# Kernel tuning notes

Hardware: AMD Instinct MI355X
Metric: run time of the kernel (lower is better)

Reference implementation:

```python
import jax, jax.numpy as jnp
import numpy as np

WIDTH = 2048
NUM_HEADS = 16
HEAD_DIM = WIDTH // NUM_HEADS  # 128
ROPE_DIMS = HEAD_DIM // 2      # 64, partial rotary
WINDOW = 512
ROPE_BASE = 10000.0
NEG_INF = -1e9


def apply_rope(x, dims, offset=0, base=ROPE_BASE):
    # x: [B, H, L, hd]; non-traditional (half-split) rotary on first `dims` dims.
    L = x.shape[2]
    half = dims // 2
    pos = (offset + jnp.arange(L)).astype(x.dtype)                     # [L]
    inv_freq = jnp.exp(-jnp.log(jnp.asarray(base, x.dtype)) * (jnp.arange(0, dims, 2).astype(x.dtype) / dims))  # [half]
    theta = pos[:, None] * inv_freq[None, :]                           # [L, half]
    cos = jnp.cos(theta)[None, None]                                   # [1,1,L,half]
    sin = jnp.sin(theta)[None, None]
    x1 = x[..., :half]
    x2 = x[..., half:dims]
    rest = x[..., dims:]
    rx1 = x1 * cos - x2 * sin
    rx2 = x1 * sin + x2 * cos
    return jnp.concatenate([rx1, rx2, rest], axis=-1)


def setup_inputs() -> dict:
    key = jax.random.key(0)
    ks = jax.random.split(key, 6)
    B, L, D, hd = 2, 2048, WIDTH, HEAD_DIM
    x = jax.random.normal(ks[0], (B, L, D), dtype=jnp.float32)
    Wq = jax.random.normal(ks[1], (D, D), dtype=jnp.float32) * 0.02
    Wk = jax.random.normal(ks[2], (D, hd), dtype=jnp.float32) * 0.02
    Wv = jax.random.normal(ks[3], (D, hd), dtype=jnp.float32) * 0.02
    Wo = jax.random.normal(ks[4], (D, D), dtype=jnp.float32) * 0.02
    bo = jax.random.normal(ks[5], (D,), dtype=jnp.float32) * 0.02
    return {"x": x, "Wq": Wq, "Wk": Wk, "Wv": Wv, "Wo": Wo, "bo": bo}


def reference(x, Wq, Wk, Wv, Wo, bo):
    B, L, D = x.shape
    H, hd = NUM_HEADS, HEAD_DIM
    scale = hd ** (-0.5)

    q = (x @ Wq).reshape(B, L, H, hd).transpose(0, 2, 1, 3)   # [B,H,L,hd]
    k = (x @ Wk).reshape(B, L, 1, hd).transpose(0, 2, 1, 3)   # [B,1,L,hd] (MQA)
    v = (x @ Wv).reshape(B, L, 1, hd).transpose(0, 2, 1, 3)

    q = apply_rope(q, ROPE_DIMS)
    k = apply_rope(k, ROPE_DIMS)

    # sliding-window causal mask: attend iff 0 <= i - j < WINDOW
    i = jnp.arange(L)[:, None]
    j = jnp.arange(L)[None, :]
    allowed = (i - j >= 0) & (i - j < WINDOW)                  # [L,L]
    mask = jnp.where(allowed, 0.0, NEG_INF).astype(x.dtype)

    scores = jnp.einsum("bhqd,bkd->bhqk", q, k[:, 0]) * scale  # [B,H,L,L]
    scores = scores + mask[None, None]
    attn = jax.nn.softmax(scores, axis=-1)
    out = jnp.einsum("bhqk,bkd->bhqd", attn, v[:, 0])          # [B,H,L,hd]
    out = out.transpose(0, 2, 1, 3).reshape(B, L, D)
    return out @ Wo + bo
```

## Files before the change

kernel.cpp:

```cpp
#include <hip/hip_runtime.h>
#include <hip/hip_bf16.h>
#include <stdint.h>


typedef float  f32x4  __attribute__((ext_vector_type(4)));
typedef __bf16 bf16x8 __attribute__((ext_vector_type(8)));

#define ASYNC_LD16(gp, lp)                                                     \
  __builtin_amdgcn_global_load_lds(                                            \
      (__attribute__((address_space(1))) void*)(gp),                           \
      (__attribute__((address_space(3))) void*)(lp), 16, 0, 0)

__global__ void cvt_bf16(const float* __restrict__ in,
                         __hip_bfloat16* __restrict__ out, int n4) {
  const int i = blockIdx.x * 256 + threadIdx.x;
  if (i >= n4) return;
  const float4 v = ((const float4*)in)[i];
  __align__(8) __hip_bfloat16 t[4] = {
      __float2bfloat16(v.x), __float2bfloat16(v.y),
      __float2bfloat16(v.z), __float2bfloat16(v.w)};
  *(uint2*)(out + (size_t)i * 4) = *(uint2*)t;
}

__global__ __launch_bounds__(256) void transpose_all(
    const float* __restrict__ Wq, const float* __restrict__ Wk,
    const float* __restrict__ Wv, const float* __restrict__ Wo,
    __hip_bfloat16* __restrict__ wqkvT, __hip_bfloat16* __restrict__ woT) {
  __shared__ float t[32][33];
  const int bid = blockIdx.x;
  const float* src;
  __hip_bfloat16* dst;
  int C, cb, rb;
  if (bid < 4096) {
    src = Wq; dst = wqkvT; C = 2048; cb = bid & 63; rb = bid >> 6;
  } else if (bid < 4352) {
    const int l = bid - 4096;
    src = Wk; dst = wqkvT + 2048ull * 2048; C = 128; cb = l & 3; rb = l >> 2;
  } else if (bid < 4608) {
    const int l = bid - 4352;
    src = Wv; dst = wqkvT + 2176ull * 2048; C = 128; cb = l & 3; rb = l >> 2;
  } else {
    const int l = bid - 4608;
    src = Wo; dst = woT; C = 2048; cb = l & 63; rb = l >> 6;
  }
  const int c0 = cb * 32, r0 = rb * 32;
  const int x = threadIdx.x & 31, y = threadIdx.x >> 5;
#pragma unroll
  for (int i = 0; i < 32; i += 8)
    t[y + i][x] = src[(size_t)(r0 + y + i) * C + c0 + x];
  __syncthreads();
#pragma unroll
  for (int i = 0; i < 32; i += 8)
    dst[(size_t)(c0 + y + i) * 2048 + r0 + x] = __float2bfloat16(t[x][y + i]);
}

__device__ __forceinline__ void gemm_core64(const __bf16* __restrict__ A,
                                            const __bf16* __restrict__ BT,
                                            int K, __bf16* As, __bf16* Bs,
                                            f32x4 (&acc)[4][4]) {
  const int tid = threadIdx.x;
  const int wave = tid >> 6;
  const int lane = tid & 63;
  const int m0 = blockIdx.y * 128;
  const int n0 = blockIdx.x * 128;
  const int wm = (wave & 1) * 64;
  const int wn = (wave >> 1) * 64;
  const int ln = lane & 15;
  const int quad = lane >> 4;
  const int rdoff = (quad ^ ((ln >> 1) & 3)) * 8;

  size_t goff[4];
  int ldsoff[4];
#pragma unroll
  for (int i = 0; i < 4; i++) {
    const int cidx = (wave * 4 + i) * 64 + lane;
    const int p = cidx >> 9;
    const int pidx = cidx & 511;
    const int row = pidx >> 2;
    const int cc = pidx & 3;
    const int cg = cc ^ ((row >> 1) & 3);
    goff[i] = (size_t)row * K + p * 32 + cg * 8;
    ldsoff[i] = (wave * 4 + i) * 512;
  }
  const __bf16* Abase = A + (size_t)m0 * K;
  const __bf16* Bbase = BT + (size_t)n0 * K;

  for (int k0 = 0; k0 < K; k0 += 64) {
#pragma unroll
    for (int i = 0; i < 4; i++)
      ASYNC_LD16(Abase + k0 + goff[i], As + ldsoff[i]);
#pragma unroll
    for (int i = 0; i < 4; i++)
      ASYNC_LD16(Bbase + k0 + goff[i], Bs + ldsoff[i]);
    __syncthreads();
    bf16x8 af[4][2], bf[4][2];
#pragma unroll
    for (int i = 0; i < 4; i++)
#pragma unroll
      for (int p = 0; p < 2; p++)
        af[i][p] = *(const bf16x8*)&As[p * 4096 + (wm + i * 16 + ln) * 32 + rdoff];
#pragma unroll
    for (int j = 0; j < 4; j++)
#pragma unroll
      for (int p = 0; p < 2; p++)
        bf[j][p] = *(const bf16x8*)&Bs[p * 4096 + (wn + j * 16 + ln) * 32 + rdoff];
#pragma unroll
    for (int p = 0; p < 2; p++)
#pragma unroll
      for (int i = 0; i < 4; i++)
#pragma unroll
        for (int j = 0; j < 4; j++)
          acc[i][j] = __builtin_amdgcn_mfma_f32_16x16x32_bf16(af[i][p], bf[j][p],
                                                              acc[i][j], 0, 0, 0);
    __syncthreads();
  }
}

__global__ __launch_bounds__(256) void gemm_qkv(
    const __bf16* __restrict__ A, const __bf16* __restrict__ BT,
    __hip_bfloat16* __restrict__ qd, __hip_bfloat16* __restrict__ kd,
    __hip_bfloat16* __restrict__ vtd, int K) {
  __shared__ __align__(16) __bf16 As[128 * 64];
  __shared__ __align__(16) __bf16 Bs[128 * 64];
  f32x4 acc[4][4];
  const f32x4 zero = {0.f, 0.f, 0.f, 0.f};
#pragma unroll
  for (int i = 0; i < 4; i++)
#pragma unroll
    for (int j = 0; j < 4; j++) acc[i][j] = zero;
  gemm_core64(A, BT, K, As, Bs, acc);

  const int tid = threadIdx.x;
  const int wave = tid >> 6;
  const int lane = tid & 63;
  const int quad = lane >> 4;
  const int ln = lane & 15;
  const int m0 = blockIdx.y * 128;
  const int n0 = blockIdx.x * 128;
  const int wm = (wave & 1) * 64;
  const int wn = (wave >> 1) * 64;

  if (n0 == 2176) {
    const int bb = m0 >> 11;
    const int mloc = m0 & 2047;
#pragma unroll
    for (int i = 0; i < 4; i++) {
      const int rb = mloc + wm + i * 16 + quad * 4;
#pragma unroll
      for (int j = 0; j < 4; j++) {
        const int col = wn + j * 16 + ln;
        __align__(8) __hip_bfloat16 t4[4];
#pragma unroll
        for (int r = 0; r < 4; r++) t4[r] = __float2bfloat16(acc[i][j][r]);
        *(uint2*)(vtd + ((size_t)(bb * 128 + col)) * 2048 + rb) = *(uint2*)t4;
      }
    }
    return;
  }

  __hip_bfloat16* dst;
  int dstride, dcol;
  if (n0 < 2048) {
    dst = qd; dstride = 2048; dcol = n0;
  } else {
    dst = kd; dstride = 128; dcol = 0;
  }
  const bool dorope = (wn == 0);
  float invf0 = 0.f, invf1 = 0.f;
  if (dorope) {
    invf0 = expf(-0.28782313662425574f * (float)ln);
    invf1 = expf(-0.28782313662425574f * (float)(16 + ln));
  }

#pragma unroll
  for (int i = 0; i < 4; i++) {
#pragma unroll
    for (int r = 0; r < 4; r++) {
      const int row = m0 + wm + i * 16 + quad * 4 + r;
      float o0 = acc[i][0][r], o1 = acc[i][1][r];
      float o2 = acc[i][2][r], o3 = acc[i][3][r];
      if (dorope) {
        const float pos = (float)(row & 2047);
        float s0, c0, s1, c1;
        __sincosf(pos * invf0, &s0, &c0);
        __sincosf(pos * invf1, &s1, &c1);
        const float a0 = o0, b0 = o2, a1 = o1, b1 = o3;
        o0 = a0 * c0 - b0 * s0;
        o2 = a0 * s0 + b0 * c0;
        o1 = a1 * c1 - b1 * s1;
        o3 = a1 * s1 + b1 * c1;
      }
      __hip_bfloat16* rp = dst + (size_t)row * dstride + dcol + wn + ln;
      rp[0]  = __float2bfloat16(o0);
      rp[16] = __float2bfloat16(o1);
      rp[32] = __float2bfloat16(o2);
      rp[48] = __float2bfloat16(o3);
    }
  }
}

__global__ __launch_bounds__(256) void gemm_out(
    const __bf16* __restrict__ A, const __bf16* __restrict__ BT,
    float* __restrict__ C, const float* __restrict__ bias, int N, int K) {
  __shared__ __align__(16) __bf16 As[128 * 64];
  __shared__ __align__(16) __bf16 Bs[128 * 64];
  f32x4 acc[4][4];
  const f32x4 zero = {0.f, 0.f, 0.f, 0.f};
#pragma unroll
  for (int i = 0; i < 4; i++)
#pragma unroll
    for (int j = 0; j < 4; j++) acc[i][j] = zero;
  gemm_core64(A, BT, K, As, Bs, acc);

  const int tid = threadIdx.x;
  const int wave = tid >> 6;
  const int lane = tid & 63;
  const int m0 = blockIdx.y * 128;
  const int n0 = blockIdx.x * 128;
  const int wm = (wave & 1) * 64;
  const int wn = (wave >> 1) * 64;
  const int lrow = lane & 15;
#pragma unroll
  for (int j = 0; j < 4; j++) {
    const int col = n0 + wn + j * 16 + lrow;
    const float bv = bias[col];
#pragma unroll
    for (int i = 0; i < 4; i++) {
#pragma unroll
      for (int r = 0; r < 4; r++) {
        const int row = m0 + wm + i * 16 + (lane >> 4) * 4 + r;
        C[(size_t)row * N + col] = acc[i][j][r] + bv;
      }
    }
  }
}

__global__ __launch_bounds__(256) void attn_mfma(
    const __bf16* __restrict__ qb,
    const __bf16* __restrict__ kb,
    const __bf16* __restrict__ vtb,
    __hip_bfloat16* __restrict__ o)
{
  __shared__ __align__(16) __bf16 Ks[4][64 * 32];
  __shared__ __align__(16) __bf16 Vs[2][128 * 32];
  __shared__ __align__(16) __bf16 Ps[4][2][2][512];
  const int tid = threadIdx.x;
  const int wave = tid >> 6;
  const int lane = tid & 63;
  const int quad = lane >> 4;
  const int ln = lane & 15;
  const int bid = blockIdx.x;
  const int q0 = (bid & 15) * 128;
  const int h = (bid >> 4) & 15;
  const int b = bid >> 8;

  bf16x8 qf[2][4];
#pragma unroll
  for (int g = 0; g < 2; g++) {
    const __bf16* qrow =
        qb + ((size_t)(b * 2048 + q0 + wave * 32 + g * 16 + ln)) * 2048 + h * 128;
#pragma unroll
    for (int ks = 0; ks < 4; ks++)
      qf[g][ks] = *(const bf16x8*)(qrow + ks * 32 + quad * 8);
  }

  f32x4 oacc[2][8];
  const f32x4 zero = {0.f, 0.f, 0.f, 0.f};
#pragma unroll
  for (int g = 0; g < 2; g++)
#pragma unroll
    for (int nb = 0; nb < 8; nb++) oacc[g][nb] = zero;
  float li[2][4] = {{0.f, 0.f, 0.f, 0.f}, {0.f, 0.f, 0.f, 0.f}};
  const float scale = 0.08838834764831845f;

  const __bf16* kbase = kb + (size_t)b * 2048 * 128;
  const __bf16* vbase = vtb + (size_t)b * 128 * 2048;

  const int tstart = (q0 >= 512) ? 0 : (512 - q0) / 64;
  for (int t = tstart; t < 10; ++t) {
    const int jt = q0 - 512 + 64 * t;
    __syncthreads();
    {
      const int key4 = lane >> 2, uu = lane & 3;
#pragma unroll
      for (int i = 0; i < 4; ++i) {
        const int c = wave * 4 + i;
        const int ks = c & 3, keybase = (c >> 2) * 16;
        ASYNC_LD16(kbase + (size_t)(jt + keybase + key4) * 128 + ks * 32 + uu * 8,
                   &Ks[ks][keybase * 32]);
      }
#pragma unroll
      for (int i = 0; i < 4; ++i) {
        const int c = wave * 4 + i;
        const int p = c & 1, dbase = (c >> 1) * 16;
        ASYNC_LD16(vbase + (size_t)(dbase + key4) * 2048 + jt + p * 32 + uu * 8,
                   &Vs[p][dbase * 32]);
      }
    }
    __syncthreads();

    f32x4 sacc[2][4];
#pragma unroll
    for (int g = 0; g < 2; g++)
#pragma unroll
      for (int j = 0; j < 4; j++) sacc[g][j] = zero;
#pragma unroll
    for (int j = 0; j < 4; j++)
#pragma unroll
      for (int ks = 0; ks < 4; ks++) {
        const bf16x8 kf = *(const bf16x8*)&Ks[ks][(j * 16 + ln) * 32 + quad * 8];
#pragma unroll
        for (int g = 0; g < 2; g++)
          sacc[g][j] = __builtin_amdgcn_mfma_f32_16x16x32_bf16(qf[g][ks], kf,
                                                               sacc[g][j], 0, 0, 0);
      }

#pragma unroll
    for (int g = 0; g < 2; g++)
#pragma unroll
      for (int j = 0; j < 4; j++)
#pragma unroll
        for (int r = 0; r < 4; r++) {
          float v = sacc[g][j][r] * scale;
          const int d0 = (wave * 32 + g * 16 + quad * 4 + r) - (j * 16 + ln);
          if (t <= 1 && d0 >= (t << 6)) v = -1e30f;
          if (t >= 8 && d0 < ((t - 8) << 6)) v = -1e30f;
          v = fminf(v, 60.f);
          const float p = __expf(v);
          li[g][r] += p;
          Ps[wave][g][j >> 1][(quad * 4 + r) * 32 + (j & 1) * 16 + ln] = (__bf16)p;
        }

    const bf16x8 pf00 = *(const bf16x8*)&Ps[wave][0][0][ln * 32 + quad * 8];
    const bf16x8 pf01 = *(const bf16x8*)&Ps[wave][0][1][ln * 32 + quad * 8];
    const bf16x8 pf10 = *(const bf16x8*)&Ps[wave][1][0][ln * 32 + quad * 8];
    const bf16x8 pf11 = *(const bf16x8*)&Ps[wave][1][1][ln * 32 + quad * 8];
#pragma unroll
    for (int nb = 0; nb < 8; nb++) {
      const bf16x8 vf0 = *(const bf16x8*)&Vs[0][(nb * 16 + ln) * 32 + quad * 8];
      const bf16x8 vf1 = *(const bf16x8*)&Vs[1][(nb * 16 + ln) * 32 + quad * 8];
      oacc[0][nb] =
          __builtin_amdgcn_mfma_f32_16x16x32_bf16(pf00, vf0, oacc[0][nb], 0, 0, 0);
      oacc[0][nb] =
          __builtin_amdgcn_mfma_f32_16x16x32_bf16(pf01, vf1, oacc[0][nb], 0, 0, 0);
      oacc[1][nb] =
          __builtin_amdgcn_mfma_f32_16x16x32_bf16(pf10, vf0, oacc[1][nb], 0, 0, 0);
      oacc[1][nb] =
          __builtin_amdgcn_mfma_f32_16x16x32_bf16(pf11, vf1, oacc[1][nb], 0, 0, 0);
    }
  }

#pragma unroll
  for (int off = 1; off < 16; off <<= 1)
#pragma unroll
    for (int g = 0; g < 2; g++)
#pragma unroll
      for (int r = 0; r < 4; r++) li[g][r] += __shfl_xor(li[g][r], off);

#pragma unroll
  for (int g = 0; g < 2; g++) {
    __hip_bfloat16* obase =
        o + ((size_t)(b * 2048 + q0 + wave * 32 + g * 16 + quad * 4)) * 2048 +
        h * 128 + ln;
#pragma unroll
    for (int r = 0; r < 4; r++) {
      const float inv = 1.0f / li[g][r];
#pragma unroll
      for (int nb = 0; nb < 8; nb++)
        obase[(size_t)r * 2048 + nb * 16] = __float2bfloat16(oacc[g][nb][r] * inv);
    }
  }
}

extern "C" void kernel_launch(void* const* d_in, const int* in_sizes, int n_in,
                              void* d_out, int out_size, void* d_ws,
                              size_t ws_size, hipStream_t stream) {
  const float* x = (const float*)d_in[0];
  const float* Wq = (const float*)d_in[1];
  const float* Wk = (const float*)d_in[2];
  const float* Wv = (const float*)d_in[3];
  const float* Wo = (const float*)d_in[4];
  const float* bo = (const float*)d_in[5];
  float* out = (float*)d_out;

  char* w = (char*)d_ws;
  auto alloc = [&](size_t bytes) {
    void* p = (void*)w;
    w += (bytes + 255) & ~(size_t)255;
    return p;
  };
  __bf16* xb = (__bf16*)alloc(4096ull * 2048 * 2);
  __hip_bfloat16* wqkvT = (__hip_bfloat16*)alloc(2304ull * 2048 * 2);
  __hip_bfloat16* woT = (__hip_bfloat16*)alloc(2048ull * 2048 * 2);
  __hip_bfloat16* qbuf = (__hip_bfloat16*)alloc(4096ull * 2048 * 2);
  __hip_bfloat16* kbuf = (__hip_bfloat16*)alloc(4096ull * 128 * 2);
  __hip_bfloat16* vtb = (__hip_bfloat16*)alloc(4096ull * 128 * 2);
  __hip_bfloat16* attnb = (__hip_bfloat16*)xb;

  cvt_bf16<<<8192, 256, 0, stream>>>(x, (__hip_bfloat16*)xb, 2097152);
  transpose_all<<<8704, 256, 0, stream>>>(Wq, Wk, Wv, Wo, wqkvT, woT);

  gemm_qkv<<<dim3(18, 32), 256, 0, stream>>>(xb, (const __bf16*)wqkvT, qbuf,
                                             kbuf, vtb, 2048);

  attn_mfma<<<512, 256, 0, stream>>>((const __bf16*)qbuf, (const __bf16*)kbuf,
                                     (const __bf16*)vtb, attnb);

  gemm_out<<<dim3(16, 32), 256, 0, stream>>>((const __bf16*)attnb,
                                             (const __bf16*)woT, out, bo, 2048,
                                             2048);
}
```

Measured before the change: 269.2 us.

## Swizzle attention LDS tiles for K, V, P and merge prep kernels

```diff
diff --git a/kernel.cpp b/kernel.cpp
--- a/kernel.cpp
+++ b/kernel.cpp
@@ -11,23 +11,23 @@
       (__attribute__((address_space(1))) void*)(gp),                           \
       (__attribute__((address_space(3))) void*)(lp), 16, 0, 0)
 
-__global__ void cvt_bf16(const float* __restrict__ in,
-                         __hip_bfloat16* __restrict__ out, int n4) {
-  const int i = blockIdx.x * 256 + threadIdx.x;
-  if (i >= n4) return;
-  const float4 v = ((const float4*)in)[i];
-  __align__(8) __hip_bfloat16 t[4] = {
-      __float2bfloat16(v.x), __float2bfloat16(v.y),
-      __float2bfloat16(v.z), __float2bfloat16(v.w)};
-  *(uint2*)(out + (size_t)i * 4) = *(uint2*)t;
-}
-
-__global__ __launch_bounds__(256) void transpose_all(
+__global__ __launch_bounds__(256) void prep_all(
+    const float* __restrict__ x, __hip_bfloat16* __restrict__ xb,
     const float* __restrict__ Wq, const float* __restrict__ Wk,
     const float* __restrict__ Wv, const float* __restrict__ Wo,
     __hip_bfloat16* __restrict__ wqkvT, __hip_bfloat16* __restrict__ woT) {
   __shared__ float t[32][33];
-  const int bid = blockIdx.x;
+  int bid = blockIdx.x;
+  if (bid < 8192) {
+    const int i = bid * 256 + threadIdx.x;
+    const float4 v = ((const float4*)x)[i];
+    __align__(8) __hip_bfloat16 o[4] = {
+        __float2bfloat16(v.x), __float2bfloat16(v.y),
+        __float2bfloat16(v.z), __float2bfloat16(v.w)};
+    *(uint2*)(xb + (size_t)i * 4) = *(uint2*)o;
+    return;
+  }
+  bid -= 8192;
   const float* src;
   __hip_bfloat16* dst;
   int C, cb, rb;
@@ -44,14 +44,14 @@
     src = Wo; dst = woT; C = 2048; cb = l & 63; rb = l >> 6;
   }
   const int c0 = cb * 32, r0 = rb * 32;
-  const int x = threadIdx.x & 31, y = threadIdx.x >> 5;
+  const int xx = threadIdx.x & 31, y = threadIdx.x >> 5;
 #pragma unroll
   for (int i = 0; i < 32; i += 8)
-    t[y + i][x] = src[(size_t)(r0 + y + i) * C + c0 + x];
+    t[y + i][xx] = src[(size_t)(r0 + y + i) * C + c0 + xx];
   __syncthreads();
 #pragma unroll
   for (int i = 0; i < 32; i += 8)
-    dst[(size_t)(c0 + y + i) * 2048 + r0 + x] = __float2bfloat16(t[x][y + i]);
+    dst[(size_t)(c0 + y + i) * 2048 + r0 + xx] = __float2bfloat16(t[xx][y + i]);
 }
 
 __device__ __forceinline__ void gemm_core64(const __bf16* __restrict__ A,
@@ -253,6 +253,8 @@
   const int q0 = (bid & 15) * 128;
   const int h = (bid >> 4) & 15;
   const int b = bid >> 8;
+  const int swr = (ln >> 1) & 3;
+  const int rdoff = (quad ^ swr) * 8;
 
   bf16x8 qf[2][4];
 #pragma unroll
@@ -282,18 +284,21 @@
     __syncthreads();
     {
       const int key4 = lane >> 2, uu = lane & 3;
+      const int sw = (key4 >> 1) & 3;
 #pragma unroll
       for (int i = 0; i < 4; ++i) {
         const int c = wave * 4 + i;
         const int ks = c & 3, keybase = (c >> 2) * 16;
-        ASYNC_LD16(kbase + (size_t)(jt + keybase + key4) * 128 + ks * 32 + uu * 8,
+        ASYNC_LD16(kbase + (size_t)(jt + keybase + key4) * 128 + ks * 32 +
+                       (uu ^ sw) * 8,
                    &Ks[ks][keybase * 32]);
       }
 #pragma unroll
       for (int i = 0; i < 4; ++i) {
         const int c = wave * 4 + i;
         const int p = c & 1, dbase = (c >> 1) * 16;
-        ASYNC_LD16(vbase + (size_t)(dbase + key4) * 2048 + jt + p * 32 + uu * 8,
+        ASYNC_LD16(vbase + (size_t)(dbase + key4) * 2048 + jt + p * 32 +
+                       (uu ^ sw) * 8,
                    &Vs[p][dbase * 32]);
       }
     }
@@ -308,7 +313,7 @@
     for (int j = 0; j < 4; j++)
 #pragma unroll
       for (int ks = 0; ks < 4; ks++) {
-        const bf16x8 kf = *(const bf16x8*)&Ks[ks][(j * 16 + ln) * 32 + quad * 8];
+        const bf16x8 kf = *(const bf16x8*)&Ks[ks][(j * 16 + ln) * 32 + rdoff];
 #pragma unroll
         for (int g = 0; g < 2; g++)
           sacc[g][j] = __builtin_amdgcn_mfma_f32_16x16x32_bf16(qf[g][ks], kf,
@@ -328,17 +333,20 @@
           v = fminf(v, 60.f);
           const float p = __expf(v);
           li[g][r] += p;
-          Ps[wave][g][j >> 1][(quad * 4 + r) * 32 + (j & 1) * 16 + ln] = (__bf16)p;
+          const int ch = (j & 1) * 2 + (ln >> 3);
+          const int swp = (quad * 2 + (r >> 1)) & 3;
+          Ps[wave][g][j >> 1]
+            [(quad * 4 + r) * 32 + (ch ^ swp) * 8 + (ln & 7)] = (__bf16)p;
         }
 
-    const bf16x8 pf00 = *(const bf16x8*)&Ps[wave][0][0][ln * 32 + quad * 8];
-    const bf16x8 pf01 = *(const bf16x8*)&Ps[wave][0][1][ln * 32 + quad * 8];
-    const bf16x8 pf10 = *(const bf16x8*)&Ps[wave][1][0][ln * 32 + quad * 8];
-    const bf16x8 pf11 = *(const bf16x8*)&Ps[wave][1][1][ln * 32 + quad * 8];
+    const bf16x8 pf00 = *(const bf16x8*)&Ps[wave][0][0][ln * 32 + rdoff];
+    const bf16x8 pf01 = *(const bf16x8*)&Ps[wave][0][1][ln * 32 + rdoff];
+    const bf16x8 pf10 = *(const bf16x8*)&Ps[wave][1][0][ln * 32 + rdoff];
+    const bf16x8 pf11 = *(const bf16x8*)&Ps[wave][1][1][ln * 32 + rdoff];
 #pragma unroll
     for (int nb = 0; nb < 8; nb++) {
-      const bf16x8 vf0 = *(const bf16x8*)&Vs[0][(nb * 16 + ln) * 32 + quad * 8];
-      const bf16x8 vf1 = *(const bf16x8*)&Vs[1][(nb * 16 + ln) * 32 + quad * 8];
+      const bf16x8 vf0 = *(const bf16x8*)&Vs[0][(nb * 16 + ln) * 32 + rdoff];
+      const bf16x8 vf1 = *(const bf16x8*)&Vs[1][(nb * 16 + ln) * 32 + rdoff];
       oacc[0][nb] =
           __builtin_amdgcn_mfma_f32_16x16x32_bf16(pf00, vf0, oacc[0][nb], 0, 0, 0);
       oacc[0][nb] =
@@ -397,8 +405,8 @@
   __hip_bfloat16* vtb = (__hip_bfloat16*)alloc(4096ull * 128 * 2);
   __hip_bfloat16* attnb = (__hip_bfloat16*)xb;
 
-  cvt_bf16<<<8192, 256, 0, stream>>>(x, (__hip_bfloat16*)xb, 2097152);
-  transpose_all<<<8704, 256, 0, stream>>>(Wq, Wk, Wv, Wo, wqkvT, woT);
+  prep_all<<<16896, 256, 0, stream>>>(x, (__hip_bfloat16*)xb, Wq, Wk, Wv, Wo,
+                                      wqkvT, woT);
 
   gemm_qkv<<<dim3(18, 32), 256, 0, stream>>>(xb, (const __bf16*)wqkvT, qbuf,
                                              kbuf, vtb, 2048);
```

New measurement: 259.7 us. 3.5% less time.
